# Kernel optimization log

Hardware: AMD Instinct MI355X
Metric: run time of the kernel (lower is better)

Reference implementation:

```python
import jax, jax.numpy as jnp
import numpy as np

N, E, IN, HID, OUT, K = 10000, 320000, 256, 256, 128, 3


def setup_inputs() -> dict:
    key = jax.random.key(0)
    ks = jax.random.split(key, 4)
    x = jax.random.normal(ks[0], (N, IN), jnp.float32)
    edge = jax.random.randint(ks[1], (2, E), 0, N)

    def glorot(k, shape):
        lim = (6.0 / (shape[-2] + shape[-1])) ** 0.5
        return jax.random.uniform(k, shape, jnp.float32, -lim, lim)

    W1 = glorot(ks[2], (K, IN, HID))
    b1 = jnp.zeros((HID,), jnp.float32)
    W2 = glorot(ks[3], (K, HID, OUT))
    b2 = jnp.zeros((OUT,), jnp.float32)
    return {"x": x, "edge": edge, "W1": W1, "b1": b1, "W2": W2, "b2": b2}


def _cheb_conv(x, src, dst, norm, W, b):
    # Chebyshev recursion: Tx_0 = x, Tx_1 = L_hat x, Tx_k = 2 L_hat Tx_{k-1} - Tx_{k-2}
    n = x.shape[0]

    def prop(t):  # sparse L_hat @ t via edge gather/scatter
        return jax.ops.segment_sum(t[src] * norm[:, None], dst, num_segments=n)

    Tx0 = x
    out = jnp.einsum('ni,io->no', Tx0, W[0])
    Tx1 = prop(Tx0)
    out = out + jnp.einsum('ni,io->no', Tx1, W[1])
    for k in range(2, W.shape[0]):
        Tx2 = 2.0 * prop(Tx1) - Tx0
        out = out + jnp.einsum('ni,io->no', Tx2, W[k])
        Tx0, Tx1 = Tx1, Tx2
    return out + b


def reference(x, edge, W1, b1, W2, b2):
    src, dst = edge[0], edge[1]
    # symmetric normalization, lambda_max = 2.0 (PyG ChebConv default):
    # L_hat = 2/lambda_max * (I - D^-1/2 A D^-1/2) - I = -D^-1/2 A D^-1/2 (zero diagonal)
    deg = jax.ops.segment_sum(jnp.ones((src.shape[0],), jnp.float32), dst, num_segments=x.shape[0])
    dis = jnp.where(deg > 0, jax.lax.rsqrt(jnp.maximum(deg, 1.0)), 0.0)
    norm = -dis[src] * dis[dst]  # [E]
    h = jax.nn.relu(_cheb_conv(x, src, dst, norm, W1, b1))
    # dropout is identity in eval mode
    return _cheb_conv(h, src, dst, norm, W2, b2)
```

## Files before the change

### kernel.cpp

```cpp
#include <hip/hip_runtime.h>


constexpr int N    = 10000;
constexpr int E    = 320000;
constexpr int KS   = 8;
constexpr int MT   = 626;
constexpr int CAP  = 96;

using bf16x8 = __attribute__((ext_vector_type(8))) short;
using f32x4  = __attribute__((ext_vector_type(4))) float;

__device__ inline float b2f(ushort u) { return __uint_as_float((unsigned)u << 16); }
__device__ inline ushort f2b(float f) {
    unsigned u = __float_as_uint(f);
    unsigned r = (u + 0x7fffu + ((u >> 16) & 1u)) >> 16;
    return (ushort)r;
}
__device__ inline size_t pidx(int r, int c) {
    return (size_t)((r >> 4) * KS + (c >> 5)) * 512 + ((c & 31) >> 3) * 128 + (r & 15) * 8 + (c & 7);
}
__device__ inline float irs(int c) { return c > 0 ? rsqrtf((float)c) : 0.f; }

__global__ void conv_all(const float* __restrict__ x,
                         const float* __restrict__ W1, const float* __restrict__ W2,
                         ushort* __restrict__ PA1, ushort* __restrict__ PA2,
                         ushort* __restrict__ PB1, ushort* __restrict__ PB2,
                         int* __restrict__ cnt) {
    int t = blockIdx.x * blockDim.x + threadIdx.x;
    if (t < N * 32) {
        if (t < 16384) cnt[t] = 0;
        int n = t >> 5, f = (t & 31) * 8;
        float4 v0 = *reinterpret_cast<const float4*>(x + (size_t)n * 256 + f);
        float4 v1 = *reinterpret_cast<const float4*>(x + (size_t)n * 256 + f + 4);
        bf16x8 o;
        o[0] = (short)f2b(v0.x); o[1] = (short)f2b(v0.y); o[2] = (short)f2b(v0.z); o[3] = (short)f2b(v0.w);
        o[4] = (short)f2b(v1.x); o[5] = (short)f2b(v1.y); o[6] = (short)f2b(v1.z); o[7] = (short)f2b(v1.w);
        *reinterpret_cast<bf16x8*>(PA1 + pidx(n, f)) = o;
        return;
    }
    t -= N * 32;
    if (t < 768 * 256) {
        int o = t % 768, i = t / 768;
        float val;
        if (o < 256)      val = W1[2 * 65536 + i * 256 + o];
        else if (o < 512) val = W1[1 * 65536 + i * 256 + (o - 256)];
        else              val = W1[i * 256 + (o - 512)] - W1[2 * 65536 + i * 256 + (o - 512)];
        PB1[pidx(o, i)] = f2b(val);
        return;
    }
    t -= 768 * 256;
    if (t < 384 * 256) {
        int o = t % 384, i = t / 384;
        float val;
        if (o < 128)      val = W2[2 * 32768 + i * 128 + o];
        else if (o < 256) val = W2[1 * 32768 + i * 128 + (o - 128)];
        else              val = W2[i * 128 + (o - 256)] - W2[2 * 32768 + i * 128 + (o - 256)];
        PB2[pidx(o, i)] = f2b(val);
        return;
    }
    t -= 384 * 256;
    if (t < 8192) {
        size_t pad = (size_t)625 * KS * 512;
        if (t < 4096) PA1[pad + t] = 0;
        else          PA2[pad + (t - 4096)] = 0;
    }
}

template<bool L2OUT>
__device__ void gemm_unit(int mt0, int ot0, int lane,
                          const ushort* __restrict__ PA, const ushort* __restrict__ PB,
                          ushort* __restrict__ out16, float* __restrict__ out32) {
    const ushort* Abase = PA + (size_t)mt0 * (KS * 512) + lane * 8;
    const ushort* Bbase = PB + (size_t)ot0 * (KS * 512) + lane * 8;

    f32x4 acc[2][6] = {};
    bf16x8 aX[2], bX[6], aY[2], bY[6];

    auto LD = [&](int ks, bf16x8 (&a)[2], bf16x8 (&b)[6]) {
#pragma unroll
        for (int mi = 0; mi < 2; ++mi)
            a[mi] = *reinterpret_cast<const bf16x8*>(Abase + (size_t)mi * (KS * 512) + ks * 512);
#pragma unroll
        for (int ni = 0; ni < 6; ++ni)
            b[ni] = *reinterpret_cast<const bf16x8*>(Bbase + (size_t)ni * (KS * 512) + ks * 512);
    };
    auto CP = [&](bf16x8 (&a)[2], bf16x8 (&b)[6]) {
#pragma unroll
        for (int mi = 0; mi < 2; ++mi)
#pragma unroll
            for (int ni = 0; ni < 6; ++ni)
                acc[mi][ni] = __builtin_amdgcn_mfma_f32_16x16x32_bf16(a[mi], b[ni], acc[mi][ni], 0, 0, 0);
    };

    LD(0, aX, bX);
#pragma unroll
    for (int ks = 0; ks < KS; ++ks) {
        if (ks & 1) { if (ks + 1 < KS) LD(ks + 1, aX, bX); CP(aY, bY); }
        else        { if (ks + 1 < KS) LD(ks + 1, aY, bY); CP(aX, bX); }
    }

    int colBase = lane & 15;
    int rowBase = (lane >> 4) * 4;
#pragma unroll
    for (int mi = 0; mi < 2; ++mi)
#pragma unroll
        for (int ni = 0; ni < 6; ++ni) {
            int col = (ot0 + ni) * 16 + colBase;
#pragma unroll
            for (int j = 0; j < 4; ++j) {
                int row = (mt0 + mi) * 16 + rowBase + j;
                if (row < N) {
                    float v = acc[mi][ni][j];
                    if (!L2OUT) {
                        out16[(size_t)row * 768 + col] = f2b(v);
                    } else {
                        if (col < 256) out16[(size_t)row * 256 + col] = f2b(v);
                        else           out32[(size_t)row * 128 + (col - 256)] = v;
                    }
                }
            }
        }
}

__global__ __launch_bounds__(256) void
sg1_kernel(const int* __restrict__ src, const int* __restrict__ dst,
           int* __restrict__ cnt, int* __restrict__ bucket,
           const ushort* __restrict__ PA, const ushort* __restrict__ PB,
           ushort* __restrict__ Z1) {
    int bid = blockIdx.x, tid = threadIdx.x;
    if (bid < 626) {
        int lane = tid & 63, wv = tid >> 6;
        int mpair = bid >> 1, half = bid & 1;
        gemm_unit<false>(mpair * 2, half * 24 + wv * 6, lane, PA, PB, Z1, nullptr);
    } else {
        int e = (bid - 626) * 256 + tid;
        int s = src[e], d = dst[e];
        int pos = atomicAdd(&cnt[d], 1);
        if (pos < CAP) bucket[(size_t)d * CAP + pos] = s;
    }
}

__global__ __launch_bounds__(256) void
gemm2_kernel(const ushort* __restrict__ PA, const ushort* __restrict__ PB,
             ushort* __restrict__ Zb, float* __restrict__ Z0f) {
    int tid = threadIdx.x, lane = tid & 63, wv = tid >> 6;
    gemm_unit<true>(blockIdx.x * 2, wv * 6, lane, PA, PB, Zb, Z0f);
}

template<int W, int MODE>
__global__ void prop(const int* __restrict__ cnt, const int* __restrict__ bucket,
                     const ushort* __restrict__ tin, int tstride,
                     const ushort* __restrict__ lin16, int lstride,
                     const float* __restrict__ lin32, const float* __restrict__ bias,
                     ushort* __restrict__ out16, float* __restrict__ out32) {
    constexpr int LPN = W / 8;
    int tid = threadIdx.x;
    int d = blockIdx.x * (256 / LPN) + tid / LPN;
    int f = (tid % LPN) * 8;
    int cd = cnt[d];
    int nE = min(cd, CAP);
    float dd = irs(cd);
    const int* bk = bucket + (size_t)d * CAP;
    const ushort* tf = tin + f;
    float accA[8] = {}, accB[8] = {};
    int i = 0;
    for (; i + 4 <= nE; i += 4) {
        int4 s4 = *reinterpret_cast<const int4*>(bk + i);
        float w0 = irs(cnt[s4.x]), w1 = irs(cnt[s4.y]), w2 = irs(cnt[s4.z]), w3 = irs(cnt[s4.w]);
        bf16x8 v0 = *reinterpret_cast<const bf16x8*>(tf + (size_t)s4.x * tstride);
        bf16x8 v1 = *reinterpret_cast<const bf16x8*>(tf + (size_t)s4.y * tstride);
        bf16x8 v2 = *reinterpret_cast<const bf16x8*>(tf + (size_t)s4.z * tstride);
        bf16x8 v3 = *reinterpret_cast<const bf16x8*>(tf + (size_t)s4.w * tstride);
#pragma unroll
        for (int j = 0; j < 8; ++j) {
            accA[j] += b2f((ushort)v0[j]) * w0 + b2f((ushort)v2[j]) * w2;
            accB[j] += b2f((ushort)v1[j]) * w1 + b2f((ushort)v3[j]) * w3;
        }
    }
    for (; i < nE; ++i) {
        int s = bk[i];
        float w = irs(cnt[s]);
        bf16x8 v0 = *reinterpret_cast<const bf16x8*>(tf + (size_t)s * tstride);
#pragma unroll
        for (int j = 0; j < 8; ++j) accA[j] += b2f((ushort)v0[j]) * w;
    }
#pragma unroll
    for (int j = 0; j < 8; ++j) accA[j] += accB[j];

    if (MODE == 0) {
        bf16x8 z = *reinterpret_cast<const bf16x8*>(lin16 + (size_t)d * lstride + f);
        bf16x8 o;
#pragma unroll
        for (int j = 0; j < 8; ++j) o[j] = (short)f2b(b2f((ushort)z[j]) - 2.f * dd * accA[j]);
        *reinterpret_cast<bf16x8*>(out16 + (size_t)d * W + f) = o;
    } else if (MODE == 1) {
        bf16x8 z = *reinterpret_cast<const bf16x8*>(lin16 + (size_t)d * lstride + f);
        bf16x8 o;
#pragma unroll
        for (int j = 0; j < 8; ++j)
            o[j] = (short)f2b(fmaxf(b2f((ushort)z[j]) + bias[f + j] - dd * accA[j], 0.f));
        *reinterpret_cast<bf16x8*>(out16 + pidx(d, f)) = o;
    } else {
        float4 z0 = *reinterpret_cast<const float4*>(lin32 + (size_t)d * W + f);
        float4 z1 = *reinterpret_cast<const float4*>(lin32 + (size_t)d * W + f + 4);
        float zz[8] = {z0.x, z0.y, z0.z, z0.w, z1.x, z1.y, z1.z, z1.w};
        float r[8];
#pragma unroll
        for (int j = 0; j < 8; ++j) r[j] = zz[j] + bias[f + j] - dd * accA[j];
        *reinterpret_cast<float4*>(out32 + (size_t)d * W + f)     = make_float4(r[0], r[1], r[2], r[3]);
        *reinterpret_cast<float4*>(out32 + (size_t)d * W + f + 4) = make_float4(r[4], r[5], r[6], r[7]);
    }
}

extern "C" void kernel_launch(void* const* d_in, const int* in_sizes, int n_in,
                              void* d_out, int out_size, void* d_ws, size_t ws_size,
                              hipStream_t stream) {
    const float* x  = (const float*)d_in[0];
    const int* edge = (const int*)d_in[1];
    const float* W1 = (const float*)d_in[2];
    const float* b1 = (const float*)d_in[3];
    const float* W2 = (const float*)d_in[4];
    const float* b2 = (const float*)d_in[5];
    const int* src = edge;
    const int* dst = edge + E;
    float* out = (float*)d_out;

    int*    cnt    = (int*)d_ws;
    int*    bucket = cnt + 16384;
    ushort* PA1 = (ushort*)(bucket + (size_t)N * CAP);
    ushort* PA2 = PA1 + (size_t)MT * KS * 512;
    ushort* PB1 = PA2 + (size_t)MT * KS * 512;
    ushort* PB2 = PB1 + (size_t)48 * KS * 512;
    ushort* Z1  = PB2 + (size_t)24 * KS * 512;
    ushort* V1  = Z1 + (size_t)N * 768;
    ushort* Zb  = V1 + (size_t)N * 256;
    ushort* V2  = Zb + (size_t)N * 256;
    float*  Z0f = (float*)(V2 + (size_t)N * 128);

    constexpr int CONV_T = N * 32 + 768 * 256 + 384 * 256 + 8192;

    conv_all<<<(CONV_T + 255) / 256, 256, 0, stream>>>(x, W1, W2, PA1, PA2, PB1, PB2, cnt);
    sg1_kernel<<<626 + 1250, 256, 0, stream>>>(src, dst, cnt, bucket, PA1, PB1, Z1);

    prop<256, 0><<<N / 8, 256, 0, stream>>>(cnt, bucket,
                                            Z1, 768, Z1 + 256, 768, nullptr, nullptr, V1, nullptr);
    prop<256, 1><<<N / 8, 256, 0, stream>>>(cnt, bucket,
                                            V1, 256, Z1 + 512, 768, nullptr, b1, PA2, nullptr);
    gemm2_kernel<<<313, 256, 0, stream>>>(PA2, PB2, Zb, Z0f);
    prop<128, 0><<<N / 16, 256, 0, stream>>>(cnt, bucket,
                                             Zb, 256, Zb + 128, 256, nullptr, nullptr, V2, nullptr);
    prop<128, 2><<<N / 16, 256, 0, stream>>>(cnt, bucket,
                                             V2, 128, nullptr, 0, Z0f, b2, nullptr, out);
}
```

Measured before the change: 115.0 us.

## Pre-scale MODE 0 outputs by source degree norm and unroll gather by 8

The MODE 0 propagation now writes its result already multiplied by the destination's inverse-sqrt degree. Later propagation passes can then sum neighbour rows without loading each neighbour's degree count and computing an rsqrt per edge. The edge loop is also unrolled from 4 to 8 neighbours, keeping more independent gathers in flight. The risk is correctness: every consumer of MODE 0 output must expect the pre-scaled values, the reordered multiply changes rounding, and the deeper unroll raises register pressure.

```diff
diff --git a/kernel.cpp b/kernel.cpp
--- a/kernel.cpp
+++ b/kernel.cpp
@@ -154,6 +154,7 @@
                      const float* __restrict__ lin32, const float* __restrict__ bias,
                      ushort* __restrict__ out16, float* __restrict__ out32) {
     constexpr int LPN = W / 8;
+    constexpr bool SC = (MODE == 0);
     int tid = threadIdx.x;
     int d = blockIdx.x * (256 / LPN) + tid / LPN;
     int f = (tid % LPN) * 8;
@@ -164,34 +165,79 @@
     const ushort* tf = tin + f;
     float accA[8] = {}, accB[8] = {};
     int i = 0;
-    for (; i + 4 <= nE; i += 4) {
+    for (; i + 8 <= nE; i += 8) {
         int4 s4 = *reinterpret_cast<const int4*>(bk + i);
-        float w0 = irs(cnt[s4.x]), w1 = irs(cnt[s4.y]), w2 = irs(cnt[s4.z]), w3 = irs(cnt[s4.w]);
+        int4 s5 = *reinterpret_cast<const int4*>(bk + i + 4);
         bf16x8 v0 = *reinterpret_cast<const bf16x8*>(tf + (size_t)s4.x * tstride);
         bf16x8 v1 = *reinterpret_cast<const bf16x8*>(tf + (size_t)s4.y * tstride);
         bf16x8 v2 = *reinterpret_cast<const bf16x8*>(tf + (size_t)s4.z * tstride);
         bf16x8 v3 = *reinterpret_cast<const bf16x8*>(tf + (size_t)s4.w * tstride);
-#pragma unroll
-        for (int j = 0; j < 8; ++j) {
-            accA[j] += b2f((ushort)v0[j]) * w0 + b2f((ushort)v2[j]) * w2;
-            accB[j] += b2f((ushort)v1[j]) * w1 + b2f((ushort)v3[j]) * w3;
+        bf16x8 v4 = *reinterpret_cast<const bf16x8*>(tf + (size_t)s5.x * tstride);
+        bf16x8 v5 = *reinterpret_cast<const bf16x8*>(tf + (size_t)s5.y * tstride);
+        bf16x8 v6 = *reinterpret_cast<const bf16x8*>(tf + (size_t)s5.z * tstride);
+        bf16x8 v7 = *reinterpret_cast<const bf16x8*>(tf + (size_t)s5.w * tstride);
+        if (SC) {
+            float w0 = irs(cnt[s4.x]), w1 = irs(cnt[s4.y]), w2 = irs(cnt[s4.z]), w3 = irs(cnt[s4.w]);
+            float w4 = irs(cnt[s5.x]), w5 = irs(cnt[s5.y]), w6 = irs(cnt[s5.z]), w7 = irs(cnt[s5.w]);
+#pragma unroll
+            for (int j = 0; j < 8; ++j) {
+                accA[j] += b2f((ushort)v0[j]) * w0 + b2f((ushort)v2[j]) * w2
+                         + b2f((ushort)v4[j]) * w4 + b2f((ushort)v6[j]) * w6;
+                accB[j] += b2f((ushort)v1[j]) * w1 + b2f((ushort)v3[j]) * w3
+                         + b2f((ushort)v5[j]) * w5 + b2f((ushort)v7[j]) * w7;
+            }
+        } else {
+#pragma unroll
+            for (int j = 0; j < 8; ++j) {
+                accA[j] += b2f((ushort)v0[j]) + b2f((ushort)v2[j])
+                         + b2f((ushort)v4[j]) + b2f((ushort)v6[j]);
+                accB[j] += b2f((ushort)v1[j]) + b2f((ushort)v3[j])
+                         + b2f((ushort)v5[j]) + b2f((ushort)v7[j]);
+            }
+        }
+    }
+    for (; i + 4 <= nE; i += 4) {
+        int4 s4 = *reinterpret_cast<const int4*>(bk + i);
+        bf16x8 v0 = *reinterpret_cast<const bf16x8*>(tf + (size_t)s4.x * tstride);
+        bf16x8 v1 = *reinterpret_cast<const bf16x8*>(tf + (size_t)s4.y * tstride);
+        bf16x8 v2 = *reinterpret_cast<const bf16x8*>(tf + (size_t)s4.z * tstride);
+        bf16x8 v3 = *reinterpret_cast<const bf16x8*>(tf + (size_t)s4.w * tstride);
+        if (SC) {
+            float w0 = irs(cnt[s4.x]), w1 = irs(cnt[s4.y]), w2 = irs(cnt[s4.z]), w3 = irs(cnt[s4.w]);
+#pragma unroll
+            for (int j = 0; j < 8; ++j) {
+                accA[j] += b2f((ushort)v0[j]) * w0 + b2f((ushort)v2[j]) * w2;
+                accB[j] += b2f((ushort)v1[j]) * w1 + b2f((ushort)v3[j]) * w3;
+            }
+        } else {
+#pragma unroll
+            for (int j = 0; j < 8; ++j) {
+                accA[j] += b2f((ushort)v0[j]) + b2f((ushort)v2[j]);
+                accB[j] += b2f((ushort)v1[j]) + b2f((ushort)v3[j]);
+            }
         }
     }
     for (; i < nE; ++i) {
         int s = bk[i];
-        float w = irs(cnt[s]);
         bf16x8 v0 = *reinterpret_cast<const bf16x8*>(tf + (size_t)s * tstride);
-#pragma unroll
-        for (int j = 0; j < 8; ++j) accA[j] += b2f((ushort)v0[j]) * w;
+        if (SC) {
+            float w = irs(cnt[s]);
+#pragma unroll
+            for (int j = 0; j < 8; ++j) accA[j] += b2f((ushort)v0[j]) * w;
+        } else {
+#pragma unroll
+            for (int j = 0; j < 8; ++j) accA[j] += b2f((ushort)v0[j]);
+        }
     }
 #pragma unroll
     for (int j = 0; j < 8; ++j) accA[j] += accB[j];
 
     if (MODE == 0) {
+        float c2 = 2.f * dd * dd;
         bf16x8 z = *reinterpret_cast<const bf16x8*>(lin16 + (size_t)d * lstride + f);
         bf16x8 o;
 #pragma unroll
-        for (int j = 0; j < 8; ++j) o[j] = (short)f2b(b2f((ushort)z[j]) - 2.f * dd * accA[j]);
+        for (int j = 0; j < 8; ++j) o[j] = (short)f2b(dd * b2f((ushort)z[j]) - c2 * accA[j]);
         *reinterpret_cast<bf16x8*>(out16 + (size_t)d * W + f) = o;
     } else if (MODE == 1) {
         bf16x8 z = *reinterpret_cast<const bf16x8*>(lin16 + (size_t)d * lstride + f);
```

New measurement: 115.5 us (median of 2 runs). Within noise of the previous version (+0.5%).

## Fuse layer-1 second propagation into layer-2 GEMM and prescale features by degree

Applied to the files above, without the earlier changes.

The second Chebyshev propagation of layer 1 (bias, ReLU) is merged with the layer-2 GEMM in one kernel. Each block gathers 32 rows into LDS and runs MFMA from there, so the packed PA2 intermediate and one launch go away. The first propagation now writes its output already multiplied by the node's inverse-sqrt degree, so later propagations skip the per-edge irs(cnt[s]) lookups. The edge-bucketing blocks are also reordered to come before the GEMM blocks in the combined launch. In exchange the fused kernel has only 313 blocks and its gather phase is serial before the GEMM, and the prescaled bf16 values round slightly differently.

```diff
diff --git a/kernel.cpp b/kernel.cpp
--- a/kernel.cpp
+++ b/kernel.cpp
@@ -23,7 +23,7 @@
 
 __global__ void conv_all(const float* __restrict__ x,
                          const float* __restrict__ W1, const float* __restrict__ W2,
-                         ushort* __restrict__ PA1, ushort* __restrict__ PA2,
+                         ushort* __restrict__ PA1,
                          ushort* __restrict__ PB1, ushort* __restrict__ PB2,
                          int* __restrict__ cnt) {
     int t = blockIdx.x * blockDim.x + threadIdx.x;
@@ -59,17 +59,15 @@
         return;
     }
     t -= 384 * 256;
-    if (t < 8192) {
+    if (t < 4096) {
         size_t pad = (size_t)625 * KS * 512;
-        if (t < 4096) PA1[pad + t] = 0;
-        else          PA2[pad + (t - 4096)] = 0;
-    }
-}
-
-template<bool L2OUT>
+        PA1[pad + t] = 0;
+    }
+}
+
 __device__ void gemm_unit(int mt0, int ot0, int lane,
                           const ushort* __restrict__ PA, const ushort* __restrict__ PB,
-                          ushort* __restrict__ out16, float* __restrict__ out32) {
+                          ushort* __restrict__ out16) {
     const ushort* Abase = PA + (size_t)mt0 * (KS * 512) + lane * 8;
     const ushort* Bbase = PB + (size_t)ot0 * (KS * 512) + lane * 8;
 
@@ -109,15 +107,8 @@
 #pragma unroll
             for (int j = 0; j < 4; ++j) {
                 int row = (mt0 + mi) * 16 + rowBase + j;
-                if (row < N) {
-                    float v = acc[mi][ni][j];
-                    if (!L2OUT) {
-                        out16[(size_t)row * 768 + col] = f2b(v);
-                    } else {
-                        if (col < 256) out16[(size_t)row * 256 + col] = f2b(v);
-                        else           out32[(size_t)row * 128 + (col - 256)] = v;
-                    }
-                }
+                if (row < N)
+                    out16[(size_t)row * 768 + col] = f2b(acc[mi][ni][j]);
             }
         }
 }
@@ -128,31 +119,24 @@
            const ushort* __restrict__ PA, const ushort* __restrict__ PB,
            ushort* __restrict__ Z1) {
     int bid = blockIdx.x, tid = threadIdx.x;
-    if (bid < 626) {
-        int lane = tid & 63, wv = tid >> 6;
-        int mpair = bid >> 1, half = bid & 1;
-        gemm_unit<false>(mpair * 2, half * 24 + wv * 6, lane, PA, PB, Z1, nullptr);
-    } else {
-        int e = (bid - 626) * 256 + tid;
+    if (bid < 1250) {
+        int e = bid * 256 + tid;
         int s = src[e], d = dst[e];
         int pos = atomicAdd(&cnt[d], 1);
         if (pos < CAP) bucket[(size_t)d * CAP + pos] = s;
-    }
-}
-
-__global__ __launch_bounds__(256) void
-gemm2_kernel(const ushort* __restrict__ PA, const ushort* __restrict__ PB,
-             ushort* __restrict__ Zb, float* __restrict__ Z0f) {
-    int tid = threadIdx.x, lane = tid & 63, wv = tid >> 6;
-    gemm_unit<true>(blockIdx.x * 2, wv * 6, lane, PA, PB, Zb, Z0f);
-}
-
-template<int W, int MODE>
-__global__ void prop(const int* __restrict__ cnt, const int* __restrict__ bucket,
-                     const ushort* __restrict__ tin, int tstride,
-                     const ushort* __restrict__ lin16, int lstride,
-                     const float* __restrict__ lin32, const float* __restrict__ bias,
-                     ushort* __restrict__ out16, float* __restrict__ out32) {
+    } else {
+        int b = bid - 1250;
+        int lane = tid & 63, wv = tid >> 6;
+        int mpair = b >> 1, half = b & 1;
+        gemm_unit(mpair * 2, half * 24 + wv * 6, lane, PA, PB, Z1);
+    }
+}
+
+template<int W>
+__global__ void propA(const int* __restrict__ cnt, const int* __restrict__ bucket,
+                      const ushort* __restrict__ tin, int tstride,
+                      const ushort* __restrict__ lin16, int lstride,
+                      ushort* __restrict__ out16) {
     constexpr int LPN = W / 8;
     int tid = threadIdx.x;
     int d = blockIdx.x * (256 / LPN) + tid / LPN;
@@ -184,32 +168,152 @@
 #pragma unroll
         for (int j = 0; j < 8; ++j) accA[j] += b2f((ushort)v0[j]) * w;
     }
-#pragma unroll
-    for (int j = 0; j < 8; ++j) accA[j] += accB[j];
-
-    if (MODE == 0) {
-        bf16x8 z = *reinterpret_cast<const bf16x8*>(lin16 + (size_t)d * lstride + f);
-        bf16x8 o;
-#pragma unroll
-        for (int j = 0; j < 8; ++j) o[j] = (short)f2b(b2f((ushort)z[j]) - 2.f * dd * accA[j]);
-        *reinterpret_cast<bf16x8*>(out16 + (size_t)d * W + f) = o;
-    } else if (MODE == 1) {
-        bf16x8 z = *reinterpret_cast<const bf16x8*>(lin16 + (size_t)d * lstride + f);
-        bf16x8 o;
-#pragma unroll
-        for (int j = 0; j < 8; ++j)
-            o[j] = (short)f2b(fmaxf(b2f((ushort)z[j]) + bias[f + j] - dd * accA[j], 0.f));
-        *reinterpret_cast<bf16x8*>(out16 + pidx(d, f)) = o;
-    } else {
-        float4 z0 = *reinterpret_cast<const float4*>(lin32 + (size_t)d * W + f);
-        float4 z1 = *reinterpret_cast<const float4*>(lin32 + (size_t)d * W + f + 4);
-        float zz[8] = {z0.x, z0.y, z0.z, z0.w, z1.x, z1.y, z1.z, z1.w};
-        float r[8];
-#pragma unroll
-        for (int j = 0; j < 8; ++j) r[j] = zz[j] + bias[f + j] - dd * accA[j];
-        *reinterpret_cast<float4*>(out32 + (size_t)d * W + f)     = make_float4(r[0], r[1], r[2], r[3]);
-        *reinterpret_cast<float4*>(out32 + (size_t)d * W + f + 4) = make_float4(r[4], r[5], r[6], r[7]);
-    }
+    float c2 = 2.f * dd * dd;
+    bf16x8 z = *reinterpret_cast<const bf16x8*>(lin16 + (size_t)d * lstride + f);
+    bf16x8 o;
+#pragma unroll
+    for (int j = 0; j < 8; ++j)
+        o[j] = (short)f2b(dd * b2f((ushort)z[j]) - c2 * (accA[j] + accB[j]));
+    *reinterpret_cast<bf16x8*>(out16 + (size_t)d * W + f) = o;
+}
+
+__global__ __launch_bounds__(256) void
+fg2_kernel(const int* __restrict__ cnt, const int* __restrict__ bucket,
+           const ushort* __restrict__ V1, const ushort* __restrict__ Z1,
+           const float* __restrict__ b1, const ushort* __restrict__ PB2,
+           ushort* __restrict__ Zb, float* __restrict__ Z0f) {
+    constexpr int LSTR = 264;
+    __shared__ ushort hl[32 * LSTR];
+    int tid = threadIdx.x;
+    int r0 = blockIdx.x * 32;
+
+    for (int pass = 0; pass < 4; ++pass) {
+        int lr = pass * 8 + tid / 32;
+        int d = r0 + lr;
+        int f = (tid % 32) * 8;
+        float acc[8] = {};
+        if (d < N) {
+            int cd = cnt[d];
+            int nE = min(cd, CAP);
+            float dd = irs(cd);
+            const int* bk = bucket + (size_t)d * CAP;
+            const ushort* tf = V1 + f;
+            float accB[8] = {};
+            int i = 0;
+            for (; i + 4 <= nE; i += 4) {
+                int4 s4 = *reinterpret_cast<const int4*>(bk + i);
+                bf16x8 v0 = *reinterpret_cast<const bf16x8*>(tf + (size_t)s4.x * 256);
+                bf16x8 v1 = *reinterpret_cast<const bf16x8*>(tf + (size_t)s4.y * 256);
+                bf16x8 v2 = *reinterpret_cast<const bf16x8*>(tf + (size_t)s4.z * 256);
+                bf16x8 v3 = *reinterpret_cast<const bf16x8*>(tf + (size_t)s4.w * 256);
+#pragma unroll
+                for (int j = 0; j < 8; ++j) {
+                    acc[j]  += b2f((ushort)v0[j]) + b2f((ushort)v2[j]);
+                    accB[j] += b2f((ushort)v1[j]) + b2f((ushort)v3[j]);
+                }
+            }
+            for (; i < nE; ++i) {
+                int s = bk[i];
+                bf16x8 v0 = *reinterpret_cast<const bf16x8*>(tf + (size_t)s * 256);
+#pragma unroll
+                for (int j = 0; j < 8; ++j) acc[j] += b2f((ushort)v0[j]);
+            }
+            bf16x8 z = *reinterpret_cast<const bf16x8*>(Z1 + (size_t)d * 768 + 512 + f);
+            bf16x8 o;
+#pragma unroll
+            for (int j = 0; j < 8; ++j)
+                o[j] = (short)f2b(fmaxf(b2f((ushort)z[j]) + b1[f + j] - dd * (acc[j] + accB[j]), 0.f));
+            *reinterpret_cast<bf16x8*>(&hl[lr * LSTR + f]) = o;
+        } else {
+            bf16x8 zr = {};
+            *reinterpret_cast<bf16x8*>(&hl[lr * LSTR + f]) = zr;
+        }
+    }
+    __syncthreads();
+
+    int lane = tid & 63, wv = tid >> 6;
+    int ot0 = wv * 6;
+    int ar = lane & 15;
+    int kh = (lane >> 4) * 8;
+    const ushort* Bbase = PB2 + (size_t)ot0 * (KS * 512) + lane * 8;
+
+    f32x4 acc[2][6] = {};
+#pragma unroll
+    for (int ks = 0; ks < KS; ++ks) {
+        bf16x8 a[2], b[6];
+#pragma unroll
+        for (int mi = 0; mi < 2; ++mi)
+            a[mi] = *reinterpret_cast<const bf16x8*>(&hl[(mi * 16 + ar) * LSTR + ks * 32 + kh]);
+#pragma unroll
+        for (int ni = 0; ni < 6; ++ni)
+            b[ni] = *reinterpret_cast<const bf16x8*>(Bbase + (size_t)ni * (KS * 512) + ks * 512);
+#pragma unroll
+        for (int mi = 0; mi < 2; ++mi)
+#pragma unroll
+            for (int ni = 0; ni < 6; ++ni)
+                acc[mi][ni] = __builtin_amdgcn_mfma_f32_16x16x32_bf16(a[mi], b[ni], acc[mi][ni], 0, 0, 0);
+    }
+
+    int colBase = lane & 15;
+    int rowBase = (lane >> 4) * 4;
+#pragma unroll
+    for (int mi = 0; mi < 2; ++mi)
+#pragma unroll
+        for (int ni = 0; ni < 6; ++ni) {
+            int col = (ot0 + ni) * 16 + colBase;
+#pragma unroll
+            for (int j = 0; j < 4; ++j) {
+                int row = r0 + mi * 16 + rowBase + j;
+                if (row < N) {
+                    float v = acc[mi][ni][j];
+                    if (col < 256) Zb[(size_t)row * 256 + col] = f2b(v);
+                    else           Z0f[(size_t)row * 128 + (col - 256)] = v;
+                }
+            }
+        }
+}
+
+__global__ void propB2(const int* __restrict__ cnt, const int* __restrict__ bucket,
+                       const ushort* __restrict__ V2,
+                       const float* __restrict__ Z0f, const float* __restrict__ b2,
+                       float* __restrict__ out) {
+    constexpr int LPN = 16;
+    int tid = threadIdx.x;
+    int d = blockIdx.x * (256 / LPN) + tid / LPN;
+    int f = (tid % LPN) * 8;
+    int cd = cnt[d];
+    int nE = min(cd, CAP);
+    float dd = irs(cd);
+    const int* bk = bucket + (size_t)d * CAP;
+    const ushort* tf = V2 + f;
+    float accA[8] = {}, accB[8] = {};
+    int i = 0;
+    for (; i + 4 <= nE; i += 4) {
+        int4 s4 = *reinterpret_cast<const int4*>(bk + i);
+        bf16x8 v0 = *reinterpret_cast<const bf16x8*>(tf + (size_t)s4.x * 128);
+        bf16x8 v1 = *reinterpret_cast<const bf16x8*>(tf + (size_t)s4.y * 128);
+        bf16x8 v2 = *reinterpret_cast<const bf16x8*>(tf + (size_t)s4.z * 128);
+        bf16x8 v3 = *reinterpret_cast<const bf16x8*>(tf + (size_t)s4.w * 128);
+#pragma unroll
+        for (int j = 0; j < 8; ++j) {
+            accA[j] += b2f((ushort)v0[j]) + b2f((ushort)v2[j]);
+            accB[j] += b2f((ushort)v1[j]) + b2f((ushort)v3[j]);
+        }
+    }
+    for (; i < nE; ++i) {
+        int s = bk[i];
+        bf16x8 v0 = *reinterpret_cast<const bf16x8*>(tf + (size_t)s * 128);
+#pragma unroll
+        for (int j = 0; j < 8; ++j) accA[j] += b2f((ushort)v0[j]);
+    }
+    float4 z0 = *reinterpret_cast<const float4*>(Z0f + (size_t)d * 128 + f);
+    float4 z1 = *reinterpret_cast<const float4*>(Z0f + (size_t)d * 128 + f + 4);
+    float zz[8] = {z0.x, z0.y, z0.z, z0.w, z1.x, z1.y, z1.z, z1.w};
+    float r[8];
+#pragma unroll
+    for (int j = 0; j < 8; ++j) r[j] = zz[j] + b2[f + j] - dd * (accA[j] + accB[j]);
+    *reinterpret_cast<float4*>(out + (size_t)d * 128 + f)     = make_float4(r[0], r[1], r[2], r[3]);
+    *reinterpret_cast<float4*>(out + (size_t)d * 128 + f + 4) = make_float4(r[4], r[5], r[6], r[7]);
 }
 
 extern "C" void kernel_launch(void* const* d_in, const int* in_sizes, int n_in,
@@ -228,8 +332,7 @@
     int*    cnt    = (int*)d_ws;
     int*    bucket = cnt + 16384;
     ushort* PA1 = (ushort*)(bucket + (size_t)N * CAP);
-    ushort* PA2 = PA1 + (size_t)MT * KS * 512;
-    ushort* PB1 = PA2 + (size_t)MT * KS * 512;
+    ushort* PB1 = PA1 + (size_t)MT * KS * 512;
     ushort* PB2 = PB1 + (size_t)48 * KS * 512;
     ushort* Z1  = PB2 + (size_t)24 * KS * 512;
     ushort* V1  = Z1 + (size_t)N * 768;
@@ -237,18 +340,13 @@
     ushort* V2  = Zb + (size_t)N * 256;
     float*  Z0f = (float*)(V2 + (size_t)N * 128);
 
-    constexpr int CONV_T = N * 32 + 768 * 256 + 384 * 256 + 8192;
-
-    conv_all<<<(CONV_T + 255) / 256, 256, 0, stream>>>(x, W1, W2, PA1, PA2, PB1, PB2, cnt);
-    sg1_kernel<<<626 + 1250, 256, 0, stream>>>(src, dst, cnt, bucket, PA1, PB1, Z1);
-
-    prop<256, 0><<<N / 8, 256, 0, stream>>>(cnt, bucket,
-                                            Z1, 768, Z1 + 256, 768, nullptr, nullptr, V1, nullptr);
-    prop<256, 1><<<N / 8, 256, 0, stream>>>(cnt, bucket,
-                                            V1, 256, Z1 + 512, 768, nullptr, b1, PA2, nullptr);
-    gemm2_kernel<<<313, 256, 0, stream>>>(PA2, PB2, Zb, Z0f);
-    prop<128, 0><<<N / 16, 256, 0, stream>>>(cnt, bucket,
-                                             Zb, 256, Zb + 128, 256, nullptr, nullptr, V2, nullptr);
-    prop<128, 2><<<N / 16, 256, 0, stream>>>(cnt, bucket,
-                                             V2, 128, nullptr, 0, Z0f, b2, nullptr, out);
-}
+    constexpr int CONV_T = N * 32 + 768 * 256 + 384 * 256 + 4096;
+
+    conv_all<<<(CONV_T + 255) / 256, 256, 0, stream>>>(x, W1, W2, PA1, PB1, PB2, cnt);
+    sg1_kernel<<<1250 + 626, 256, 0, stream>>>(src, dst, cnt, bucket, PA1, PB1, Z1);
+
+    propA<256><<<N / 8, 256, 0, stream>>>(cnt, bucket, Z1, 768, Z1 + 256, 768, V1);
+    fg2_kernel<<<(N + 31) / 32, 256, 0, stream>>>(cnt, bucket, V1, Z1, b1, PB2, Zb, Z0f);
+    propA<128><<<N / 16, 256, 0, stream>>>(cnt, bucket, Zb, 256, Zb + 128, 256, V2);
+    propB2<<<N / 16, 256, 0, stream>>>(cnt, bucket, V2, Z0f, b2, out);
+}
```

After: 131.0 us. +13.9%, slower.

## Bucket edges by source chunk and prescale intermediates by source degree

Applied to the files above, without the earlier changes.

Each destination's neighbor list is split into 4 buckets keyed by source-index range. The propagation kernels then walk the sources one range at a time, so concurrent threads hit a smaller, cache-resident slice of the feature array. The first propagation of each layer now writes its output already scaled by the node's inverse-sqrt degree, which lets the second propagation skip the per-edge degree lookup and rsqrt. The edge-bucketing blocks are also placed before the GEMM blocks in the fused launch. The cost is a larger bucket array, extra per-cell counters and atomics, and a fixed per-cell capacity of 40 that would drop edges if a source range ever exceeds it.

```diff
diff --git a/kernel.cpp b/kernel.cpp
--- a/kernel.cpp
+++ b/kernel.cpp
@@ -5,7 +5,8 @@
 constexpr int E    = 320000;
 constexpr int KS   = 8;
 constexpr int MT   = 626;
-constexpr int CAP  = 96;
+constexpr int CHK  = 4;
+constexpr int CAP2 = 40;
 
 using bf16x8 = __attribute__((ext_vector_type(8))) short;
 using f32x4  = __attribute__((ext_vector_type(4))) float;
@@ -25,10 +26,11 @@
                          const float* __restrict__ W1, const float* __restrict__ W2,
                          ushort* __restrict__ PA1, ushort* __restrict__ PA2,
                          ushort* __restrict__ PB1, ushort* __restrict__ PB2,
-                         int* __restrict__ cnt) {
+                         int* __restrict__ cnt, int* __restrict__ cnt2) {
     int t = blockIdx.x * blockDim.x + threadIdx.x;
     if (t < N * 32) {
         if (t < 16384) cnt[t] = 0;
+        else if (t < 16384 + CHK * N) cnt2[t - 16384] = 0;
         int n = t >> 5, f = (t & 31) * 8;
         float4 v0 = *reinterpret_cast<const float4*>(x + (size_t)n * 256 + f);
         float4 v1 = *reinterpret_cast<const float4*>(x + (size_t)n * 256 + f + 4);
@@ -124,19 +126,23 @@
 
 __global__ __launch_bounds__(256) void
 sg1_kernel(const int* __restrict__ src, const int* __restrict__ dst,
-           int* __restrict__ cnt, int* __restrict__ bucket,
+           int* __restrict__ cnt, int* __restrict__ cnt2, int* __restrict__ bucket2,
            const ushort* __restrict__ PA, const ushort* __restrict__ PB,
            ushort* __restrict__ Z1) {
     int bid = blockIdx.x, tid = threadIdx.x;
-    if (bid < 626) {
+    if (bid < 1250) {
+        int e = bid * 256 + tid;
+        int s = src[e], d = dst[e];
+        atomicAdd(&cnt[d], 1);
+        int c = (unsigned)s / 2500;
+        int cell = d * CHK + c;
+        int pos = atomicAdd(&cnt2[cell], 1);
+        if (pos < CAP2) bucket2[(size_t)cell * CAP2 + pos] = s;
+    } else {
+        int b = bid - 1250;
         int lane = tid & 63, wv = tid >> 6;
-        int mpair = bid >> 1, half = bid & 1;
+        int mpair = b >> 1, half = b & 1;
         gemm_unit<false>(mpair * 2, half * 24 + wv * 6, lane, PA, PB, Z1, nullptr);
-    } else {
-        int e = (bid - 626) * 256 + tid;
-        int s = src[e], d = dst[e];
-        int pos = atomicAdd(&cnt[d], 1);
-        if (pos < CAP) bucket[(size_t)d * CAP + pos] = s;
     }
 }
 
@@ -148,50 +154,70 @@
 }
 
 template<int W, int MODE>
-__global__ void prop(const int* __restrict__ cnt, const int* __restrict__ bucket,
+__global__ void prop(const int* __restrict__ cnt, const int* __restrict__ cnt2,
+                     const int* __restrict__ bucket2,
                      const ushort* __restrict__ tin, int tstride,
                      const ushort* __restrict__ lin16, int lstride,
                      const float* __restrict__ lin32, const float* __restrict__ bias,
                      ushort* __restrict__ out16, float* __restrict__ out32) {
     constexpr int LPN = W / 8;
+    constexpr bool SC = (MODE == 0);
     int tid = threadIdx.x;
     int d = blockIdx.x * (256 / LPN) + tid / LPN;
     int f = (tid % LPN) * 8;
-    int cd = cnt[d];
-    int nE = min(cd, CAP);
-    float dd = irs(cd);
-    const int* bk = bucket + (size_t)d * CAP;
+    float dd = irs(cnt[d]);
     const ushort* tf = tin + f;
     float accA[8] = {}, accB[8] = {};
-    int i = 0;
-    for (; i + 4 <= nE; i += 4) {
-        int4 s4 = *reinterpret_cast<const int4*>(bk + i);
-        float w0 = irs(cnt[s4.x]), w1 = irs(cnt[s4.y]), w2 = irs(cnt[s4.z]), w3 = irs(cnt[s4.w]);
-        bf16x8 v0 = *reinterpret_cast<const bf16x8*>(tf + (size_t)s4.x * tstride);
-        bf16x8 v1 = *reinterpret_cast<const bf16x8*>(tf + (size_t)s4.y * tstride);
-        bf16x8 v2 = *reinterpret_cast<const bf16x8*>(tf + (size_t)s4.z * tstride);
-        bf16x8 v3 = *reinterpret_cast<const bf16x8*>(tf + (size_t)s4.w * tstride);
-#pragma unroll
-        for (int j = 0; j < 8; ++j) {
-            accA[j] += b2f((ushort)v0[j]) * w0 + b2f((ushort)v2[j]) * w2;
-            accB[j] += b2f((ushort)v1[j]) * w1 + b2f((ushort)v3[j]) * w3;
+
+    for (int c = 0; c < CHK; ++c) {
+        int cell = d * CHK + c;
+        int nE = min(cnt2[cell], CAP2);
+        const int* bk = bucket2 + (size_t)cell * CAP2;
+        int i = 0;
+        for (; i + 4 <= nE; i += 4) {
+            int4 s4 = *reinterpret_cast<const int4*>(bk + i);
+            bf16x8 v0 = *reinterpret_cast<const bf16x8*>(tf + (size_t)s4.x * tstride);
+            bf16x8 v1 = *reinterpret_cast<const bf16x8*>(tf + (size_t)s4.y * tstride);
+            bf16x8 v2 = *reinterpret_cast<const bf16x8*>(tf + (size_t)s4.z * tstride);
+            bf16x8 v3 = *reinterpret_cast<const bf16x8*>(tf + (size_t)s4.w * tstride);
+            if (SC) {
+                float w0 = irs(cnt[s4.x]), w1 = irs(cnt[s4.y]);
+                float w2 = irs(cnt[s4.z]), w3 = irs(cnt[s4.w]);
+#pragma unroll
+                for (int j = 0; j < 8; ++j) {
+                    accA[j] += b2f((ushort)v0[j]) * w0 + b2f((ushort)v2[j]) * w2;
+                    accB[j] += b2f((ushort)v1[j]) * w1 + b2f((ushort)v3[j]) * w3;
+                }
+            } else {
+#pragma unroll
+                for (int j = 0; j < 8; ++j) {
+                    accA[j] += b2f((ushort)v0[j]) + b2f((ushort)v2[j]);
+                    accB[j] += b2f((ushort)v1[j]) + b2f((ushort)v3[j]);
+                }
+            }
         }
-    }
-    for (; i < nE; ++i) {
-        int s = bk[i];
-        float w = irs(cnt[s]);
-        bf16x8 v0 = *reinterpret_cast<const bf16x8*>(tf + (size_t)s * tstride);
-#pragma unroll
-        for (int j = 0; j < 8; ++j) accA[j] += b2f((ushort)v0[j]) * w;
+        for (; i < nE; ++i) {
+            int s = bk[i];
+            bf16x8 v0 = *reinterpret_cast<const bf16x8*>(tf + (size_t)s * tstride);
+            if (SC) {
+                float w = irs(cnt[s]);
+#pragma unroll
+                for (int j = 0; j < 8; ++j) accA[j] += b2f((ushort)v0[j]) * w;
+            } else {
+#pragma unroll
+                for (int j = 0; j < 8; ++j) accA[j] += b2f((ushort)v0[j]);
+            }
+        }
     }
 #pragma unroll
     for (int j = 0; j < 8; ++j) accA[j] += accB[j];
 
     if (MODE == 0) {
+        float c2 = 2.f * dd * dd;
         bf16x8 z = *reinterpret_cast<const bf16x8*>(lin16 + (size_t)d * lstride + f);
         bf16x8 o;
 #pragma unroll
-        for (int j = 0; j < 8; ++j) o[j] = (short)f2b(b2f((ushort)z[j]) - 2.f * dd * accA[j]);
+        for (int j = 0; j < 8; ++j) o[j] = (short)f2b(dd * b2f((ushort)z[j]) - c2 * accA[j]);
         *reinterpret_cast<bf16x8*>(out16 + (size_t)d * W + f) = o;
     } else if (MODE == 1) {
         bf16x8 z = *reinterpret_cast<const bf16x8*>(lin16 + (size_t)d * lstride + f);
@@ -225,9 +251,10 @@
     const int* dst = edge + E;
     float* out = (float*)d_out;
 
-    int*    cnt    = (int*)d_ws;
-    int*    bucket = cnt + 16384;
-    ushort* PA1 = (ushort*)(bucket + (size_t)N * CAP);
+    int*    cnt     = (int*)d_ws;
+    int*    cnt2    = cnt + 16384;
+    int*    bucket2 = cnt2 + 40960;
+    ushort* PA1 = (ushort*)(bucket2 + (size_t)N * CHK * CAP2);
     ushort* PA2 = PA1 + (size_t)MT * KS * 512;
     ushort* PB1 = PA2 + (size_t)MT * KS * 512;
     ushort* PB2 = PB1 + (size_t)48 * KS * 512;
@@ -239,16 +266,16 @@
 
     constexpr int CONV_T = N * 32 + 768 * 256 + 384 * 256 + 8192;
 
-    conv_all<<<(CONV_T + 255) / 256, 256, 0, stream>>>(x, W1, W2, PA1, PA2, PB1, PB2, cnt);
-    sg1_kernel<<<626 + 1250, 256, 0, stream>>>(src, dst, cnt, bucket, PA1, PB1, Z1);
-
-    prop<256, 0><<<N / 8, 256, 0, stream>>>(cnt, bucket,
+    conv_all<<<(CONV_T + 255) / 256, 256, 0, stream>>>(x, W1, W2, PA1, PA2, PB1, PB2, cnt, cnt2);
+    sg1_kernel<<<1250 + 626, 256, 0, stream>>>(src, dst, cnt, cnt2, bucket2, PA1, PB1, Z1);
+
+    prop<256, 0><<<N / 8, 256, 0, stream>>>(cnt, cnt2, bucket2,
                                             Z1, 768, Z1 + 256, 768, nullptr, nullptr, V1, nullptr);
-    prop<256, 1><<<N / 8, 256, 0, stream>>>(cnt, bucket,
+    prop<256, 1><<<N / 8, 256, 0, stream>>>(cnt, cnt2, bucket2,
                                             V1, 256, Z1 + 512, 768, nullptr, b1, PA2, nullptr);
     gemm2_kernel<<<313, 256, 0, stream>>>(PA2, PB2, Zb, Z0f);
-    prop<128, 0><<<N / 16, 256, 0, stream>>>(cnt, bucket,
+    prop<128, 0><<<N / 16, 256, 0, stream>>>(cnt, cnt2, bucket2,
                                              Zb, 256, Zb + 128, 256, nullptr, nullptr, V2, nullptr);
-    prop<128, 2><<<N / 16, 256, 0, stream>>>(cnt, bucket,
+    prop<128, 2><<<N / 16, 256, 0, stream>>>(cnt, cnt2, bucket2,
                                              V2, 128, nullptr, 0, Z0f, b2, nullptr, out);
 }
```

After: 145.0 us. 1.26x slower.
